# Kernel tuning notes

Hardware: AMD Instinct MI355X
Metric: run time of the kernel (lower is better)

The kernel has to match this reference:

```python
import jax, jax.numpy as jnp
import numpy as np

B, S, D, H = 4, 1024, 1024, 16
DK = D // H
NEG = -1e9


def setup_inputs() -> dict:
    key = jax.random.key(0)
    ks = jax.random.split(key, 14)
    sc = 1.0 / np.sqrt(D)
    inp = {
        "query": jax.random.normal(ks[0], (B, S, D), jnp.float32),
        "key": jax.random.normal(ks[1], (B, S, D), jnp.float32),
        "value": jax.random.normal(ks[2], (B, S, D), jnp.float32),
        "mask": jax.random.randint(ks[3], (B, S, S), 0, 2, jnp.int32),
        "group_prob": jax.random.uniform(ks[4], (B, S, S), jnp.float32),
        "Wq": jax.random.normal(ks[5], (D, D), jnp.float32) * sc,
        "bq": jnp.zeros((D,), jnp.float32),
        "Wk": jax.random.normal(ks[6], (D, D), jnp.float32) * sc,
        "bk": jnp.zeros((D,), jnp.float32),
        "Wv": jax.random.normal(ks[7], (D, D), jnp.float32) * sc,
        "bv": jnp.zeros((D,), jnp.float32),
        "Wo": jax.random.normal(ks[8], (D, D), jnp.float32) * sc,
        "bo": jnp.zeros((D,), jnp.float32),
    }
    return inp


def reference(query, key, value, mask, group_prob, Wq, bq, Wk, bk, Wv, bv, Wo, bo):
    # QKV projections, split heads: [B,S,D] -> [B,H,S,DK]
    def proj(x, W, b):
        return (x @ W.T + b).reshape(B, S, H, DK).transpose(0, 2, 1, 3)

    q = proj(query, Wq, bq)
    k = proj(key, Wk, bk)
    v = proj(value, Wv, bv)

    scores = jnp.einsum("bhqd,bhkd->bhqk", q, k) / jnp.sqrt(jnp.float32(DK))

    # group_prob branch: allowed where mask OR diagonal is nonzero
    diag = jnp.eye(S, dtype=jnp.int32)
    allowed = (mask[:, None, :, :] | diag[None, None, :, :]) != 0  # [B,1,S,S]
    scores = jnp.where(allowed, scores, NEG)

    p_attn = jax.nn.softmax(scores, axis=-1)
    p_attn = p_attn * group_prob[:, None, :, :]  # post-softmax group reweighting

    x = jnp.einsum("bhqk,bhkd->bhqd", p_attn, v)
    x = x.transpose(0, 2, 1, 3).reshape(B, S, D)
    return x @ Wo.T + bo
```

## Files before the change

kernel.cpp:

```cpp
#include <hip/hip_runtime.h>
#include <hip/hip_bf16.h>


typedef __attribute__((ext_vector_type(8))) __bf16 bf16x8;
typedef __attribute__((ext_vector_type(4))) float f32x4;
typedef __attribute__((ext_vector_type(8))) unsigned short u16x8;

#define GSTR 40

__device__ __forceinline__ bf16x8 lds_read8(const unsigned short* p) {
  bf16x8 r;
  __builtin_memcpy(&r, __builtin_assume_aligned(p, 16), 16);
  return r;
}
__device__ __forceinline__ void lds_write8(unsigned short* p, const void* v) {
  __builtin_memcpy(__builtin_assume_aligned(p, 16), v, 16);
}
__device__ __forceinline__ void cvt8n(const float4 a, const float4 b, u16x8* hi, u16x8* lo) {
  const float fv[8] = {a.x, a.y, a.z, a.w, b.x, b.y, b.z, b.w};
  union { u16x8 v; __bf16 e[8]; } hh, ll;
#pragma unroll
  for (int i = 0; i < 8; ++i) {
    const __bf16 h = (__bf16)fv[i];
    hh.e[i] = h;
    ll.e[i] = (__bf16)(fv[i] - (float)h);
  }
  *hi = hh.v; *lo = ll.v;
}
__device__ __forceinline__ unsigned short bfbits(float f) {
  const __bf16 h = (__bf16)f;
  unsigned short u; __builtin_memcpy(&u, &h, 2); return u;
}

__global__ __launch_bounds__(256) void k_gemm(
    const float* __restrict__ X0, const float* __restrict__ X1, const float* __restrict__ X2,
    const float* __restrict__ W0, const float* __restrict__ W1, const float* __restrict__ W2,
    const float* __restrict__ B0, const float* __restrict__ B1, const float* __restrict__ B2,
    float* __restrict__ O0, float* __restrict__ O1, float* __restrict__ O2)
{
  const int z = blockIdx.z;
  const float* X = (z == 0) ? X0 : (z == 1) ? X1 : X2;
  const float* W = (z == 0) ? W0 : (z == 1) ? W1 : W2;
  const float* Bi = (z == 0) ? B0 : (z == 1) ? B1 : B2;
  float* O = (z == 0) ? O0 : (z == 1) ? O1 : O2;

  const int bid = blockIdx.x;
  const int swz = (bid & 7) * 64 + (bid >> 3);
  const int n0 = (swz & 15) * 64, m0 = (swz >> 4) * 128;

  __shared__ alignas(16) unsigned short Ah[128 * GSTR], Al[128 * GSTR];
  __shared__ alignas(16) unsigned short Bh[64 * GSTR], Bl[64 * GSTR];
  const int tid = threadIdx.x, l = tid & 63, w = tid >> 6;
  const int wr = w >> 1, wc = w & 1;

  f32x4 acc[4][2];
#pragma unroll
  for (int i = 0; i < 4; ++i)
#pragma unroll
    for (int j = 0; j < 2; ++j) acc[i][j] = (f32x4){0.f, 0.f, 0.f, 0.f};

  const int arow = tid >> 1, ac0 = (tid & 1) * 16;
  const int brow = tid >> 2, bc0 = (tid & 3) * 8;
  const float* xsrc = X + (size_t)(m0 + arow) * 1024 + ac0;
  const float* wsrc = W + (size_t)(n0 + brow) * 1024 + bc0;

  float4 fx[4], fw[2];
#pragma unroll
  for (int i = 0; i < 4; ++i) fx[i] = *(const float4*)(xsrc + i * 4);
#pragma unroll
  for (int i = 0; i < 2; ++i) fw[i] = *(const float4*)(wsrc + i * 4);

  for (int kt = 0; kt < 32; ++kt) {
    u16x8 xh[2], xl[2], wh1, wl1;
    cvt8n(fx[0], fx[1], &xh[0], &xl[0]);
    cvt8n(fx[2], fx[3], &xh[1], &xl[1]);
    cvt8n(fw[0], fw[1], &wh1, &wl1);
    if (kt < 31) {
      const float* nx = xsrc + (kt + 1) * 32;
      const float* nw = wsrc + (kt + 1) * 32;
#pragma unroll
      for (int i = 0; i < 4; ++i) fx[i] = *(const float4*)(nx + i * 4);
#pragma unroll
      for (int i = 0; i < 2; ++i) fw[i] = *(const float4*)(nw + i * 4);
    }
    __syncthreads();
#pragma unroll
    for (int hf = 0; hf < 2; ++hf) {
      lds_write8(&Ah[arow * GSTR + ac0 + hf * 8], &xh[hf]);
      lds_write8(&Al[arow * GSTR + ac0 + hf * 8], &xl[hf]);
    }
    lds_write8(&Bh[brow * GSTR + bc0], &wh1);
    lds_write8(&Bl[brow * GSTR + bc0], &wl1);
    __syncthreads();

    bf16x8 ah[4], al[4], bh[2], bl[2];
#pragma unroll
    for (int mf = 0; mf < 4; ++mf) {
      const int r = wr * 64 + mf * 16 + (l & 15);
      ah[mf] = lds_read8(&Ah[r * GSTR + (l >> 4) * 8]);
      al[mf] = lds_read8(&Al[r * GSTR + (l >> 4) * 8]);
    }
#pragma unroll
    for (int nf = 0; nf < 2; ++nf) {
      const int r = wc * 32 + nf * 16 + (l & 15);
      bh[nf] = lds_read8(&Bh[r * GSTR + (l >> 4) * 8]);
      bl[nf] = lds_read8(&Bl[r * GSTR + (l >> 4) * 8]);
    }
#pragma unroll
    for (int mf = 0; mf < 4; ++mf)
#pragma unroll
      for (int nf = 0; nf < 2; ++nf) {
        acc[mf][nf] = __builtin_amdgcn_mfma_f32_16x16x32_bf16(ah[mf], bh[nf], acc[mf][nf], 0, 0, 0);
        acc[mf][nf] = __builtin_amdgcn_mfma_f32_16x16x32_bf16(ah[mf], bl[nf], acc[mf][nf], 0, 0, 0);
        acc[mf][nf] = __builtin_amdgcn_mfma_f32_16x16x32_bf16(al[mf], bh[nf], acc[mf][nf], 0, 0, 0);
      }
  }

#pragma unroll
  for (int nf = 0; nf < 2; ++nf) {
    const int col = n0 + wc * 32 + nf * 16 + (l & 15);
    const float bias = Bi[col];
#pragma unroll
    for (int mf = 0; mf < 4; ++mf) {
      const int rbase = m0 + wr * 64 + mf * 16 + (l >> 4) * 4;
#pragma unroll
      for (int j = 0; j < 4; ++j)
        O[(size_t)(rbase + j) * 1024 + col] = acc[mf][nf][j] + bias;
    }
  }
}

__global__ __launch_bounds__(256) void k_attn(
    const float* Qp, const float* __restrict__ Kp, const float* __restrict__ Vp,
    const int* __restrict__ Mask, const float* __restrict__ Gp,
    float* Xo)
{
  const int h = blockIdx.x, qt = blockIdx.y, b = blockIdx.z;
  __shared__ alignas(16) unsigned short Kh[64 * 64], Vh[64 * 64], Ph[64 * 64];
  const int tid = threadIdx.x, l = tid & 63, w = tid >> 6;

  const float* kbase = Kp + (size_t)b * 1048576 + h * 64;
  const float* vbase = Vp + (size_t)b * 1048576 + h * 64;

  bf16x8 aq[2];
  {
    const int qrow = qt * 64 + w * 16 + (l & 15);
    const float* qp_ = Qp + ((size_t)(b * 1024 + qrow)) * 1024 + h * 64;
#pragma unroll
    for (int ks = 0; ks < 2; ++ks) {
      const float4 t0 = *(const float4*)(qp_ + ks * 32 + (l >> 4) * 8);
      const float4 t1 = *(const float4*)(qp_ + ks * 32 + (l >> 4) * 8 + 4);
      const float fv[8] = {t0.x, t0.y, t0.z, t0.w, t1.x, t1.y, t1.z, t1.w};
      union { bf16x8 v; __bf16 e[8]; } hh;
#pragma unroll
      for (int i = 0; i < 8; ++i) hh.e[i] = (__bf16)fv[i];
      aq[ks] = hh.v;
    }
  }

  f32x4 accO[4];
#pragma unroll
  for (int nf = 0; nf < 4; ++nf) accO[nf] = (f32x4){0.f, 0.f, 0.f, 0.f};
  float zacc[4] = {0.f, 0.f, 0.f, 0.f};

  const int qloc0 = w * 16 + (l >> 4) * 4;
  const int qg0 = qt * 64 + qloc0;
  const int mcol = l & 15;

  const int krow = tid >> 2, kd0 = (tid & 3) * 16;
  const int kb4 = (tid & 15) * 4, db4 = (tid >> 4) * 4;

  float4 kreg[4], vreg[4];
  {
    const float* ks_ = kbase + (size_t)krow * 1024 + kd0;
#pragma unroll
    for (int i = 0; i < 4; ++i) kreg[i] = *(const float4*)(ks_ + i * 4);
    const float* vs_ = vbase + (size_t)kb4 * 1024 + db4;
#pragma unroll
    for (int i = 0; i < 4; ++i) vreg[i] = *(const float4*)(vs_ + (size_t)i * 1024);
  }

  for (int kt = 0; kt < 16; ++kt) {
    __syncthreads();

    int mk[4][4]; float gv[4][4];
#pragma unroll
    for (int nf = 0; nf < 4; ++nf) {
      const int kg = kt * 64 + nf * 16 + mcol;
#pragma unroll
      for (int j = 0; j < 4; ++j) {
        const size_t roff = ((size_t)(b * 1024 + qg0 + j)) << 10;
        mk[nf][j] = Mask[roff + kg];
        gv[nf][j] = Gp[roff + kg];
      }
    }

    {
      const float kf[16] = {kreg[0].x, kreg[0].y, kreg[0].z, kreg[0].w,
                            kreg[1].x, kreg[1].y, kreg[1].z, kreg[1].w,
                            kreg[2].x, kreg[2].y, kreg[2].z, kreg[2].w,
                            kreg[3].x, kreg[3].y, kreg[3].z, kreg[3].w};
#pragma unroll
      for (int hf = 0; hf < 2; ++hf) {
        union { u16x8 v; __bf16 e[8]; } hh;
#pragma unroll
        for (int i = 0; i < 8; ++i) hh.e[i] = (__bf16)kf[hf * 8 + i];
        const int c = (kd0 + hf * 8) ^ ((krow & 7) << 3);
        lds_write8(&Kh[krow * 64 + c], &hh.v);
      }
    }
    {
      const float col[4][4] = {{vreg[0].x, vreg[1].x, vreg[2].x, vreg[3].x},
                               {vreg[0].y, vreg[1].y, vreg[2].y, vreg[3].y},
                               {vreg[0].z, vreg[1].z, vreg[2].z, vreg[3].z},
                               {vreg[0].w, vreg[1].w, vreg[2].w, vreg[3].w}};
#pragma unroll
      for (int i = 0; i < 4; ++i) {
        const int d = db4 + i;
        union { __bf16 e[4]; unsigned long long v; } pk;
#pragma unroll
        for (int u = 0; u < 4; ++u) pk.e[u] = (__bf16)col[i][u];
        const int c = kb4 ^ ((d & 7) << 3);
        __builtin_memcpy(__builtin_assume_aligned(&Vh[d * 64 + c], 8), &pk.v, 8);
      }
    }
    if (kt < 15) {
      const float* ks_ = kbase + (size_t)((kt + 1) * 64 + krow) * 1024 + kd0;
#pragma unroll
      for (int i = 0; i < 4; ++i) kreg[i] = *(const float4*)(ks_ + i * 4);
      const float* vs_ = vbase + (size_t)((kt + 1) * 64 + kb4) * 1024 + db4;
#pragma unroll
      for (int i = 0; i < 4; ++i) vreg[i] = *(const float4*)(vs_ + (size_t)i * 1024);
    }
    __syncthreads();

#pragma unroll
    for (int nf = 0; nf < 4; ++nf) {
      f32x4 sacc = (f32x4){0.f, 0.f, 0.f, 0.f};
      const int kr = nf * 16 + (l & 15);
#pragma unroll
      for (int ks = 0; ks < 2; ++ks) {
        const int c = (ks * 32 + (l >> 4) * 8) ^ ((kr & 7) << 3);
        sacc = __builtin_amdgcn_mfma_f32_16x16x32_bf16(aq[ks], lds_read8(&Kh[kr * 64 + c]), sacc, 0, 0, 0);
      }
      const int kg = kt * 64 + nf * 16 + mcol;
#pragma unroll
      for (int j = 0; j < 4; ++j) {
        const int qg = qg0 + j;
        const int allowed = mk[nf][j] | (qg == kg);
        const float e = allowed ? exp2f(fmaf(sacc[j], 0.18033688f, -17.31234049f)) : 0.f;
        zacc[j] += e;
        const int qloc = qloc0 + j;
        Ph[qloc * 64 + ((nf * 16 + mcol) ^ ((qloc & 7) << 3))] = bfbits(e * gv[nf][j]);
      }
    }
    bf16x8 pah[2];
    {
      const int ar = w * 16 + (l & 15);
#pragma unroll
      for (int ks = 0; ks < 2; ++ks) {
        const int c = (ks * 32 + (l >> 4) * 8) ^ ((ar & 7) << 3);
        pah[ks] = lds_read8(&Ph[ar * 64 + c]);
      }
    }
#pragma unroll
    for (int nf = 0; nf < 4; ++nf) {
      const int dr = nf * 16 + (l & 15);
#pragma unroll
      for (int ks = 0; ks < 2; ++ks) {
        const int c = (ks * 32 + (l >> 4) * 8) ^ ((dr & 7) << 3);
        accO[nf] = __builtin_amdgcn_mfma_f32_16x16x32_bf16(pah[ks], lds_read8(&Vh[dr * 64 + c]), accO[nf], 0, 0, 0);
      }
    }
  }

#pragma unroll
  for (int j = 0; j < 4; ++j) {
#pragma unroll
    for (int off = 1; off < 16; off <<= 1) zacc[j] += __shfl_xor(zacc[j], off, 64);
  }
  float rz[4];
#pragma unroll
  for (int j = 0; j < 4; ++j) rz[j] = 1.f / zacc[j];

#pragma unroll
  for (int nf = 0; nf < 4; ++nf) {
    const int d = nf * 16 + (l & 15);
#pragma unroll
    for (int j = 0; j < 4; ++j) {
      const int qg = qg0 + j;
      Xo[((size_t)(b * 1024 + qg)) * 1024 + h * 64 + d] = accO[nf][j] * rz[j];
    }
  }
}

extern "C" void kernel_launch(void* const* d_in, const int* in_sizes, int n_in,
                              void* d_out, int out_size, void* d_ws, size_t ws_size,
                              hipStream_t stream) {
  const float* query = (const float*)d_in[0];
  const float* key_in = (const float*)d_in[1];
  const float* value = (const float*)d_in[2];
  const int* mask = (const int*)d_in[3];
  const float* gp = (const float*)d_in[4];
  const float* Wq = (const float*)d_in[5];
  const float* bq = (const float*)d_in[6];
  const float* Wk = (const float*)d_in[7];
  const float* bk = (const float*)d_in[8];
  const float* Wv = (const float*)d_in[9];
  const float* bv = (const float*)d_in[10];
  const float* Wo = (const float*)d_in[11];
  const float* bo = (const float*)d_in[12];
  float* out = (float*)d_out;

  float* kp = (float*)d_ws;
  float* vp = kp + 4194304;
  float* qp = vp + 4194304;
  float* xo = qp;

  hipLaunchKernelGGL(k_gemm, dim3(512, 1, 3), dim3(256), 0, stream,
                     query, key_in, value, Wq, Wk, Wv, bq, bk, bv, qp, kp, vp);
  hipLaunchKernelGGL(k_attn, dim3(16, 16, 4), dim3(256), 0, stream,
                     qp, kp, vp, mask, gp, xo);
  hipLaunchKernelGGL(k_gemm, dim3(512, 1, 1), dim3(256), 0, stream,
                     xo, xo, xo, Wo, Wo, Wo, bo, bo, bo, out, out, out);
}
```

Baseline: 218.0 us.

## Drop split-bf16 compensation in QKV GEMM, add dedicated smaller-tile output GEMM

```diff
diff --git a/kernel.cpp b/kernel.cpp
--- a/kernel.cpp
+++ b/kernel.cpp
@@ -6,7 +6,7 @@
 typedef __attribute__((ext_vector_type(4))) float f32x4;
 typedef __attribute__((ext_vector_type(8))) unsigned short u16x8;
 
-#define GSTR 40
+#define RS 72
 
 __device__ __forceinline__ bf16x8 lds_read8(const unsigned short* p) {
   bf16x8 r;
@@ -16,7 +16,14 @@
 __device__ __forceinline__ void lds_write8(unsigned short* p, const void* v) {
   __builtin_memcpy(__builtin_assume_aligned(p, 16), v, 16);
 }
-__device__ __forceinline__ void cvt8n(const float4 a, const float4 b, u16x8* hi, u16x8* lo) {
+__device__ __forceinline__ u16x8 cvt8h(const float4 a, const float4 b) {
+  const float fv[8] = {a.x, a.y, a.z, a.w, b.x, b.y, b.z, b.w};
+  union { u16x8 v; __bf16 e[8]; } hh;
+#pragma unroll
+  for (int i = 0; i < 8; ++i) hh.e[i] = (__bf16)fv[i];
+  return hh.v;
+}
+__device__ __forceinline__ void cvt8hl(const float4 a, const float4 b, u16x8* hi, u16x8* lo) {
   const float fv[8] = {a.x, a.y, a.z, a.w, b.x, b.y, b.z, b.w};
   union { u16x8 v; __bf16 e[8]; } hh, ll;
 #pragma unroll
@@ -32,7 +39,7 @@
   unsigned short u; __builtin_memcpy(&u, &h, 2); return u;
 }
 
-__global__ __launch_bounds__(256) void k_gemm(
+__global__ __launch_bounds__(256) void k_gemm_qkv(
     const float* __restrict__ X0, const float* __restrict__ X1, const float* __restrict__ X2,
     const float* __restrict__ W0, const float* __restrict__ W1, const float* __restrict__ W2,
     const float* __restrict__ B0, const float* __restrict__ B1, const float* __restrict__ B2,
@@ -48,8 +55,8 @@
   const int swz = (bid & 7) * 64 + (bid >> 3);
   const int n0 = (swz & 15) * 64, m0 = (swz >> 4) * 128;
 
-  __shared__ alignas(16) unsigned short Ah[128 * GSTR], Al[128 * GSTR];
-  __shared__ alignas(16) unsigned short Bh[64 * GSTR], Bl[64 * GSTR];
+  __shared__ alignas(16) unsigned short Ah[128 * RS];
+  __shared__ alignas(16) unsigned short Bh[64 * RS];
   const int tid = threadIdx.x, l = tid & 63, w = tid >> 6;
   const int wr = w >> 1, wc = w & 1;
 
@@ -59,61 +66,60 @@
 #pragma unroll
     for (int j = 0; j < 2; ++j) acc[i][j] = (f32x4){0.f, 0.f, 0.f, 0.f};
 
-  const int arow = tid >> 1, ac0 = (tid & 1) * 16;
-  const int brow = tid >> 2, bc0 = (tid & 3) * 8;
+  const int arow = tid >> 1, ac0 = (tid & 1) * 32;
+  const int brow = tid >> 2, bc0 = (tid & 3) * 16;
   const float* xsrc = X + (size_t)(m0 + arow) * 1024 + ac0;
   const float* wsrc = W + (size_t)(n0 + brow) * 1024 + bc0;
 
-  float4 fx[4], fw[2];
-#pragma unroll
-  for (int i = 0; i < 4; ++i) fx[i] = *(const float4*)(xsrc + i * 4);
-#pragma unroll
-  for (int i = 0; i < 2; ++i) fw[i] = *(const float4*)(wsrc + i * 4);
-
-  for (int kt = 0; kt < 32; ++kt) {
-    u16x8 xh[2], xl[2], wh1, wl1;
-    cvt8n(fx[0], fx[1], &xh[0], &xl[0]);
-    cvt8n(fx[2], fx[3], &xh[1], &xl[1]);
-    cvt8n(fw[0], fw[1], &wh1, &wl1);
-    if (kt < 31) {
-      const float* nx = xsrc + (kt + 1) * 32;
-      const float* nw = wsrc + (kt + 1) * 32;
-#pragma unroll
-      for (int i = 0; i < 4; ++i) fx[i] = *(const float4*)(nx + i * 4);
-#pragma unroll
-      for (int i = 0; i < 2; ++i) fw[i] = *(const float4*)(nw + i * 4);
-    }
-    __syncthreads();
-#pragma unroll
-    for (int hf = 0; hf < 2; ++hf) {
-      lds_write8(&Ah[arow * GSTR + ac0 + hf * 8], &xh[hf]);
-      lds_write8(&Al[arow * GSTR + ac0 + hf * 8], &xl[hf]);
-    }
-    lds_write8(&Bh[brow * GSTR + bc0], &wh1);
-    lds_write8(&Bl[brow * GSTR + bc0], &wl1);
-    __syncthreads();
-
-    bf16x8 ah[4], al[4], bh[2], bl[2];
+  float4 fx[8], fw[4];
+#pragma unroll
+  for (int i = 0; i < 8; ++i) fx[i] = *(const float4*)(xsrc + i * 4);
+#pragma unroll
+  for (int i = 0; i < 4; ++i) fw[i] = *(const float4*)(wsrc + i * 4);
+
+  for (int kt = 0; kt < 16; ++kt) {
+    u16x8 xh[4], wh2[2];
+#pragma unroll
+    for (int g = 0; g < 4; ++g) xh[g] = cvt8h(fx[2 * g], fx[2 * g + 1]);
+#pragma unroll
+    for (int g = 0; g < 2; ++g) wh2[g] = cvt8h(fw[2 * g], fw[2 * g + 1]);
+    if (kt < 15) {
+      const float* nx = xsrc + (kt + 1) * 64;
+      const float* nw = wsrc + (kt + 1) * 64;
+#pragma unroll
+      for (int i = 0; i < 8; ++i) fx[i] = *(const float4*)(nx + i * 4);
+#pragma unroll
+      for (int i = 0; i < 4; ++i) fw[i] = *(const float4*)(nw + i * 4);
+    }
+    __syncthreads();
+#pragma unroll
+    for (int g = 0; g < 4; ++g) lds_write8(&Ah[arow * RS + ac0 + g * 8], &xh[g]);
+#pragma unroll
+    for (int g = 0; g < 2; ++g) lds_write8(&Bh[brow * RS + bc0 + g * 8], &wh2[g]);
+    __syncthreads();
+
+    bf16x8 ah[4][2], bh[2][2];
 #pragma unroll
     for (int mf = 0; mf < 4; ++mf) {
       const int r = wr * 64 + mf * 16 + (l & 15);
-      ah[mf] = lds_read8(&Ah[r * GSTR + (l >> 4) * 8]);
-      al[mf] = lds_read8(&Al[r * GSTR + (l >> 4) * 8]);
+#pragma unroll
+      for (int ks = 0; ks < 2; ++ks)
+        ah[mf][ks] = lds_read8(&Ah[r * RS + ks * 32 + (l >> 4) * 8]);
     }
 #pragma unroll
     for (int nf = 0; nf < 2; ++nf) {
       const int r = wc * 32 + nf * 16 + (l & 15);
-      bh[nf] = lds_read8(&Bh[r * GSTR + (l >> 4) * 8]);
-      bl[nf] = lds_read8(&Bl[r * GSTR + (l >> 4) * 8]);
+#pragma unroll
+      for (int ks = 0; ks < 2; ++ks)
+        bh[nf][ks] = lds_read8(&Bh[r * RS + ks * 32 + (l >> 4) * 8]);
     }
 #pragma unroll
     for (int mf = 0; mf < 4; ++mf)
 #pragma unroll
-      for (int nf = 0; nf < 2; ++nf) {
-        acc[mf][nf] = __builtin_amdgcn_mfma_f32_16x16x32_bf16(ah[mf], bh[nf], acc[mf][nf], 0, 0, 0);
-        acc[mf][nf] = __builtin_amdgcn_mfma_f32_16x16x32_bf16(ah[mf], bl[nf], acc[mf][nf], 0, 0, 0);
-        acc[mf][nf] = __builtin_amdgcn_mfma_f32_16x16x32_bf16(al[mf], bh[nf], acc[mf][nf], 0, 0, 0);
-      }
+      for (int nf = 0; nf < 2; ++nf)
+#pragma unroll
+        for (int ks = 0; ks < 2; ++ks)
+          acc[mf][nf] = __builtin_amdgcn_mfma_f32_16x16x32_bf16(ah[mf][ks], bh[nf][ks], acc[mf][nf], 0, 0, 0);
   }
 
 #pragma unroll
@@ -126,6 +132,103 @@
 #pragma unroll
       for (int j = 0; j < 4; ++j)
         O[(size_t)(rbase + j) * 1024 + col] = acc[mf][nf][j] + bias;
+    }
+  }
+}
+
+__global__ __launch_bounds__(256) void k_gemm_out(
+    const float* __restrict__ X, const float* __restrict__ W,
+    const float* __restrict__ Bi, float* __restrict__ Out)
+{
+  const int bid = blockIdx.x;
+  const int swz = (bid & 7) * 128 + (bid >> 3);
+  const int n0 = (swz & 15) * 64, m0 = (swz >> 4) * 64;
+
+  __shared__ alignas(16) unsigned short Ah[64 * RS];
+  __shared__ alignas(16) unsigned short Bh[64 * RS], Bl[64 * RS];
+  const int tid = threadIdx.x, l = tid & 63, w = tid >> 6;
+  const int wr = w >> 1, wc = w & 1;
+
+  f32x4 acc[2][2];
+#pragma unroll
+  for (int i = 0; i < 2; ++i)
+#pragma unroll
+    for (int j = 0; j < 2; ++j) acc[i][j] = (f32x4){0.f, 0.f, 0.f, 0.f};
+
+  const int srow = tid >> 2, sc0 = (tid & 3) * 16;
+  const float* xsrc = X + (size_t)(m0 + srow) * 1024 + sc0;
+  const float* wsrc = W + (size_t)(n0 + srow) * 1024 + sc0;
+
+  float4 fx[4], fw[4];
+#pragma unroll
+  for (int i = 0; i < 4; ++i) {
+    fx[i] = *(const float4*)(xsrc + i * 4);
+    fw[i] = *(const float4*)(wsrc + i * 4);
+  }
+
+  for (int kt = 0; kt < 16; ++kt) {
+    u16x8 xh[2], wh2[2], wl2[2];
+#pragma unroll
+    for (int g = 0; g < 2; ++g) {
+      xh[g] = cvt8h(fx[2 * g], fx[2 * g + 1]);
+      cvt8hl(fw[2 * g], fw[2 * g + 1], &wh2[g], &wl2[g]);
+    }
+    if (kt < 15) {
+      const float* nx = xsrc + (kt + 1) * 64;
+      const float* nw = wsrc + (kt + 1) * 64;
+#pragma unroll
+      for (int i = 0; i < 4; ++i) {
+        fx[i] = *(const float4*)(nx + i * 4);
+        fw[i] = *(const float4*)(nw + i * 4);
+      }
+    }
+    __syncthreads();
+#pragma unroll
+    for (int g = 0; g < 2; ++g) {
+      lds_write8(&Ah[srow * RS + sc0 + g * 8], &xh[g]);
+      lds_write8(&Bh[srow * RS + sc0 + g * 8], &wh2[g]);
+      lds_write8(&Bl[srow * RS + sc0 + g * 8], &wl2[g]);
+    }
+    __syncthreads();
+
+    bf16x8 ah[2][2], bh[2][2], bl[2][2];
+#pragma unroll
+    for (int mf = 0; mf < 2; ++mf) {
+      const int r = wr * 32 + mf * 16 + (l & 15);
+#pragma unroll
+      for (int ks = 0; ks < 2; ++ks)
+        ah[mf][ks] = lds_read8(&Ah[r * RS + ks * 32 + (l >> 4) * 8]);
+    }
+#pragma unroll
+    for (int nf = 0; nf < 2; ++nf) {
+      const int r = wc * 32 + nf * 16 + (l & 15);
+#pragma unroll
+      for (int ks = 0; ks < 2; ++ks) {
+        bh[nf][ks] = lds_read8(&Bh[r * RS + ks * 32 + (l >> 4) * 8]);
+        bl[nf][ks] = lds_read8(&Bl[r * RS + ks * 32 + (l >> 4) * 8]);
+      }
+    }
+#pragma unroll
+    for (int mf = 0; mf < 2; ++mf)
+#pragma unroll
+      for (int nf = 0; nf < 2; ++nf)
+#pragma unroll
+        for (int ks = 0; ks < 2; ++ks) {
+          acc[mf][nf] = __builtin_amdgcn_mfma_f32_16x16x32_bf16(ah[mf][ks], bh[nf][ks], acc[mf][nf], 0, 0, 0);
+          acc[mf][nf] = __builtin_amdgcn_mfma_f32_16x16x32_bf16(ah[mf][ks], bl[nf][ks], acc[mf][nf], 0, 0, 0);
+        }
+  }
+
+#pragma unroll
+  for (int nf = 0; nf < 2; ++nf) {
+    const int col = n0 + wc * 32 + nf * 16 + (l & 15);
+    const float bias = Bi[col];
+#pragma unroll
+    for (int mf = 0; mf < 2; ++mf) {
+      const int rbase = m0 + wr * 32 + mf * 16 + (l >> 4) * 4;
+#pragma unroll
+      for (int j = 0; j < 4; ++j)
+        Out[(size_t)(rbase + j) * 1024 + col] = acc[mf][nf][j] + bias;
     }
   }
 }
@@ -150,11 +253,7 @@
     for (int ks = 0; ks < 2; ++ks) {
       const float4 t0 = *(const float4*)(qp_ + ks * 32 + (l >> 4) * 8);
       const float4 t1 = *(const float4*)(qp_ + ks * 32 + (l >> 4) * 8 + 4);
-      const float fv[8] = {t0.x, t0.y, t0.z, t0.w, t1.x, t1.y, t1.z, t1.w};
-      union { bf16x8 v; __bf16 e[8]; } hh;
-#pragma unroll
-      for (int i = 0; i < 8; ++i) hh.e[i] = (__bf16)fv[i];
-      aq[ks] = hh.v;
+      aq[ks] = (bf16x8)cvt8h(t0, t1);
     }
   }
 
@@ -196,18 +295,12 @@
     }
 
     {
-      const float kf[16] = {kreg[0].x, kreg[0].y, kreg[0].z, kreg[0].w,
-                            kreg[1].x, kreg[1].y, kreg[1].z, kreg[1].w,
-                            kreg[2].x, kreg[2].y, kreg[2].z, kreg[2].w,
-                            kreg[3].x, kreg[3].y, kreg[3].z, kreg[3].w};
-#pragma unroll
-      for (int hf = 0; hf < 2; ++hf) {
-        union { u16x8 v; __bf16 e[8]; } hh;
-#pragma unroll
-        for (int i = 0; i < 8; ++i) hh.e[i] = (__bf16)kf[hf * 8 + i];
-        const int c = (kd0 + hf * 8) ^ ((krow & 7) << 3);
-        lds_write8(&Kh[krow * 64 + c], &hh.v);
-      }
+      u16x8 h0 = cvt8h(kreg[0], kreg[1]);
+      u16x8 h1 = cvt8h(kreg[2], kreg[3]);
+      const int c0 = kd0 ^ ((krow & 7) << 3);
+      const int c1 = (kd0 + 8) ^ ((krow & 7) << 3);
+      lds_write8(&Kh[krow * 64 + c0], &h0);
+      lds_write8(&Kh[krow * 64 + c1], &h1);
     }
     {
       const float col[4][4] = {{vreg[0].x, vreg[1].x, vreg[2].x, vreg[3].x},
@@ -317,10 +410,10 @@
   float* qp = vp + 4194304;
   float* xo = qp;
 
-  hipLaunchKernelGGL(k_gemm, dim3(512, 1, 3), dim3(256), 0, stream,
+  hipLaunchKernelGGL(k_gemm_qkv, dim3(512, 1, 3), dim3(256), 0, stream,
                      query, key_in, value, Wq, Wk, Wv, bq, bk, bv, qp, kp, vp);
   hipLaunchKernelGGL(k_attn, dim3(16, 16, 4), dim3(256), 0, stream,
                      qp, kp, vp, mask, gp, xo);
-  hipLaunchKernelGGL(k_gemm, dim3(512, 1, 1), dim3(256), 0, stream,
-                     xo, xo, xo, Wo, Wo, Wo, bo, bo, bo, out, out, out);
-}
+  hipLaunchKernelGGL(k_gemm_out, dim3(1024), dim3(256), 0, stream,
+                     xo, Wo, bo, out);
+}
```

Measured after the change: 252.2 us. +15.7%, slower.
